# Optimization experiments

Measured on AMD Instinct MI355X. Metric: run time of the kernel, lower is better.

The kernel has to match this reference:

```python
import jax, jax.numpy as jnp
import numpy as np
import math

HIDDEN = 1024
N_HEADS = 16
N_KV = 4
HEAD_DIM = HIDDEN // N_HEADS  # 64
B, S = 2, 2048
THETA = 100000.0


def _freqs_cos_sin(dim, end, theta):
    # yarn params: original_max_position_embeddings=2048 >= end, so no ramp scaling,
    # attention_factor=1.0 -> plain RoPE frequencies.
    inv = 1.0 / theta ** (np.arange(0, dim, 2)[: dim // 2] / dim)
    t = np.arange(end)
    f = np.outer(t, inv).astype(np.float32)  # (end, dim/2)
    cos = np.concatenate([np.cos(f), np.cos(f)], axis=-1)  # (end, dim)
    sin = np.concatenate([np.sin(f), np.sin(f)], axis=-1)
    return jnp.asarray(cos), jnp.asarray(sin)


def _rotate(x):
    # stack([-x[...,1::2], x[...,::2]], -1).reshape_as(x)
    return jnp.stack([-x[..., 1::2], x[..., ::2]], axis=-1).reshape(x.shape)


def setup_inputs() -> dict:
    key = jax.random.key(0)
    ks = jax.random.split(key, 9)
    s = 0.02
    return {
        "hidden_states": jax.random.normal(ks[0], (B, S, HIDDEN), jnp.float32),
        "attention_mask": jnp.ones((B, S), jnp.int32),
        "Wq": jax.random.normal(ks[1], (HIDDEN, HIDDEN), jnp.float32) * s,
        "bq": jnp.zeros((HIDDEN,), jnp.float32),
        "Wk": jax.random.normal(ks[2], (HIDDEN, N_KV * HEAD_DIM), jnp.float32) * s,
        "bk": jnp.zeros((N_KV * HEAD_DIM,), jnp.float32),
        "Wv": jax.random.normal(ks[3], (HIDDEN, N_KV * HEAD_DIM), jnp.float32) * s,
        "bv": jnp.zeros((N_KV * HEAD_DIM,), jnp.float32),
        "Wo": jax.random.normal(ks[4], (HIDDEN, HIDDEN), jnp.float32) * s,
        "bo": jnp.zeros((HIDDEN,), jnp.float32),
    }


def reference(hidden_states, attention_mask, Wq, bq, Wk, bk, Wv, bv, Wo, bo):
    b, s, _ = hidden_states.shape
    q = (hidden_states @ Wq + bq).reshape(b, s, N_HEADS, HEAD_DIM)
    k = (hidden_states @ Wk + bk).reshape(b, s, N_KV, HEAD_DIM)
    v = (hidden_states @ Wv + bv).reshape(b, s, N_KV, HEAD_DIM)

    cos, sin = _freqs_cos_sin(HEAD_DIM, s, THETA)
    cos = cos[:, None, :]  # (s,1,d) broadcasts over (b,s,h,d)
    sin = sin[:, None, :]
    q = q * cos + _rotate(q) * sin
    k = k * cos + _rotate(k) * sin

    # GQA: repeat_interleave kv heads -> jnp.repeat along head axis
    rep = N_HEADS // N_KV
    k = jnp.repeat(k, rep, axis=2)
    v = jnp.repeat(v, rep, axis=2)

    scores = jnp.einsum("bqhd,bkhd->bhqk", q, k) / math.sqrt(HEAD_DIM)
    neg = jnp.finfo(scores.dtype).min
    causal = jnp.triu(jnp.ones((s, s), bool), k=1)  # (q,kv)
    bias = jnp.where(causal, neg, 0.0).astype(scores.dtype)[None, None]
    key_mask = attention_mask.astype(bool)[:, None, None, :]  # (b,1,1,kv)
    bias = jnp.where(key_mask, bias, neg)
    probs = jax.nn.softmax(scores + bias, axis=-1)
    attn = jnp.einsum("bhqk,bkhd->bqhd", probs, v).reshape(b, s, HIDDEN)
    return attn @ Wo + bo
```

## Files before the change

kernel.cpp:

```cpp
#include <hip/hip_runtime.h>
#include <cstddef>
#include <cstdint>

#define B_   2
#define S_   2048
#define HID  1024
#define NH_  16
#define NKV_ 4
#define DH_  64
#define ROWS (B_ * S_)
#define NQKV 1536
#define QSCALE 0.18033688011112042f

typedef __bf16 bf16_t;
typedef _Float16 f16_t;
typedef bf16_t bf16x8 __attribute__((ext_vector_type(8)));
typedef bf16_t bf16x4 __attribute__((ext_vector_type(4)));
typedef f16_t  f16x8  __attribute__((ext_vector_type(8)));
typedef f16_t  f16x4  __attribute__((ext_vector_type(4)));
typedef float  f32x4  __attribute__((ext_vector_type(4)));

typedef __attribute__((address_space(1))) const uint32_t gu32_t;
typedef __attribute__((address_space(3))) uint32_t lu32_t;

__device__ __forceinline__ void gl_lds16(const void* g, void* l) {
  __builtin_amdgcn_global_load_lds((gu32_t*)g, (lu32_t*)l, 16, 0, 0);
}

__global__ void prep_all(const float* __restrict__ hs,
                         const float* __restrict__ Wq, const float* __restrict__ Wk,
                         const float* __restrict__ Wv, const float* __restrict__ Wo,
                         const float* __restrict__ bq, const float* __restrict__ bk,
                         const float* __restrict__ bv,
                         bf16_t* __restrict__ hsb,
                         bf16_t* __restrict__ Wt, bf16_t* __restrict__ Wot,
                         float* __restrict__ ball, float2* __restrict__ lut)
{
  const int bid = blockIdx.x;
  if (bid < 2048) {
    const int i = (bid * 256 + threadIdx.x) * 8;
    float4 a = *(const float4*)(hs + i);
    float4 b = *(const float4*)(hs + i + 4);
    bf16x8 o;
    o[0]=(bf16_t)a.x; o[1]=(bf16_t)a.y; o[2]=(bf16_t)a.z; o[3]=(bf16_t)a.w;
    o[4]=(bf16_t)b.x; o[5]=(bf16_t)b.y; o[6]=(bf16_t)b.z; o[7]=(bf16_t)b.w;
    *(bf16x8*)(hsb + i) = o;
    return;
  }
  if (bid >= 4614) {
    const int idx = (bid - 4614) * 256 + threadIdx.x;
    const int s = idx >> 5, j = idx & 31;
    const float L = 0.51905126482615037f;
    const float ang = (float)s * exp2f(-L * (float)j);
    lut[idx] = make_float2(cosf(ang), sinf(ang));
    return;
  }
  if (bid >= 4608) {
    int i = (bid - 4608) * 256 + threadIdx.x;
    if (i < NQKV) ball[i] = (i < 1024) ? bq[i] : ((i < 1280) ? bk[i-1024] : bv[i-1280]);
    return;
  }
  const int wb = bid - 2048;
  const float* src; bf16_t* dst; int N, n0, k0;
  if (wb < 1024)      { src = Wq; dst = Wt;            N = 1024; int t = wb;      n0=(t&31)*32; k0=(t>>5)*32; }
  else if (wb < 1280) { src = Wk; dst = Wt + 1024*HID; N = 256;  int t = wb-1024; n0=(t&7)*32;  k0=(t>>3)*32; }
  else if (wb < 1536) { src = Wv; dst = Wt + 1280*HID; N = 256;  int t = wb-1280; n0=(t&7)*32;  k0=(t>>3)*32; }
  else                { src = Wo; dst = Wot;           N = 1024; int t = wb-1536; n0=(t&31)*32; k0=(t>>5)*32; }
  __shared__ bf16_t T[32][33];
  const int tx = threadIdx.x & 31, ty = threadIdx.x >> 5;
#pragma unroll
  for (int i = 0; i < 4; ++i)
    T[ty + i*8][tx] = (bf16_t)src[(size_t)(k0 + ty + i*8) * N + n0 + tx];
  __syncthreads();
#pragma unroll
  for (int i = 0; i < 4; ++i)
    dst[(size_t)(n0 + ty + i*8) * HID + k0 + tx] = T[tx][ty + i*8];
}

__global__ __launch_bounds__(256, 3) void gemm64_b16o(
    const bf16_t* __restrict__ A, const bf16_t* __restrict__ Bt,
    const float* __restrict__ bias, bf16_t* __restrict__ C, int N)
{
  __shared__ bf16_t As[128 * 64];
  __shared__ bf16_t Bs[64 * 64];
  const int tid  = threadIdx.x;
  const int w    = tid >> 6;
  const int lane = tid & 63;
  const int m    = lane & 15;
  const int quad = lane >> 4;
  const int wm   = w >> 1, wn = w & 1;
  const size_t bm = (size_t)blockIdx.y * 128;
  const size_t bn = (size_t)blockIdx.x * 64;

  const int srow = w * 8 + (lane >> 3);
  const int scol = (lane & 7) * 8;
  const bf16_t* Ag = A  + (bm + srow) * HID + scol;
  const bf16_t* Bg = Bt + (bn + srow) * HID + scol;

  f32x4 acc[4][2];
#pragma unroll
  for (int i = 0; i < 4; ++i)
#pragma unroll
    for (int j = 0; j < 2; ++j) acc[i][j] = (f32x4){0.f, 0.f, 0.f, 0.f};

  for (int k0 = 0; k0 < HID; k0 += 64) {
    __syncthreads();
#pragma unroll
    for (int i = 0; i < 4; ++i)
      gl_lds16(Ag + (size_t)(i * 32) * HID + k0, &As[(w * 8 + i * 32) * 64]);
#pragma unroll
    for (int i = 0; i < 2; ++i)
      gl_lds16(Bg + (size_t)(i * 32) * HID + k0, &Bs[(w * 8 + i * 32) * 64]);
    __syncthreads();
#pragma unroll
    for (int ks = 0; ks < 2; ++ks) {
      bf16x8 af[4], bfr[2];
#pragma unroll
      for (int mt = 0; mt < 4; ++mt)
        af[mt] = *(const bf16x8*)&As[(wm * 64 + mt * 16 + m) * 64 + ks * 32 + quad * 8];
#pragma unroll
      for (int nt = 0; nt < 2; ++nt)
        bfr[nt] = *(const bf16x8*)&Bs[(wn * 32 + nt * 16 + m) * 64 + ks * 32 + quad * 8];
#pragma unroll
      for (int mt = 0; mt < 4; ++mt)
#pragma unroll
        for (int nt = 0; nt < 2; ++nt)
          acc[mt][nt] = __builtin_amdgcn_mfma_f32_16x16x32_bf16(bfr[nt], af[mt], acc[mt][nt], 0, 0, 0);
    }
  }
#pragma unroll
  for (int mt = 0; mt < 4; ++mt) {
    const size_t row = bm + wm * 64 + mt * 16 + m;
#pragma unroll
    for (int nt = 0; nt < 2; ++nt) {
      const size_t col = bn + wn * 32 + nt * 16 + quad * 4;
      float4 bb = *(const float4*)&bias[col];
      bf16x4 o;
      o[0] = (bf16_t)(acc[mt][nt][0] + bb.x);
      o[1] = (bf16_t)(acc[mt][nt][1] + bb.y);
      o[2] = (bf16_t)(acc[mt][nt][2] + bb.z);
      o[3] = (bf16_t)(acc[mt][nt][3] + bb.w);
      *(bf16x4*)&C[row * N + col] = o;
    }
  }
}

__global__ __launch_bounds__(256, 3) void gemm64_f32o(
    const bf16_t* __restrict__ A, const bf16_t* __restrict__ Bt,
    const float* __restrict__ bias, float* __restrict__ C, int N)
{
  __shared__ bf16_t As[128 * 64];
  __shared__ bf16_t Bs[64 * 64];
  const int tid  = threadIdx.x;
  const int w    = tid >> 6;
  const int lane = tid & 63;
  const int m    = lane & 15;
  const int quad = lane >> 4;
  const int wm   = w >> 1, wn = w & 1;
  const size_t bm = (size_t)blockIdx.y * 128;
  const size_t bn = (size_t)blockIdx.x * 64;

  const int srow = w * 8 + (lane >> 3);
  const int scol = (lane & 7) * 8;
  const bf16_t* Ag = A  + (bm + srow) * HID + scol;
  const bf16_t* Bg = Bt + (bn + srow) * HID + scol;

  f32x4 acc[4][2];
#pragma unroll
  for (int i = 0; i < 4; ++i)
#pragma unroll
    for (int j = 0; j < 2; ++j) acc[i][j] = (f32x4){0.f, 0.f, 0.f, 0.f};

  for (int k0 = 0; k0 < HID; k0 += 64) {
    __syncthreads();
#pragma unroll
    for (int i = 0; i < 4; ++i)
      gl_lds16(Ag + (size_t)(i * 32) * HID + k0, &As[(w * 8 + i * 32) * 64]);
#pragma unroll
    for (int i = 0; i < 2; ++i)
      gl_lds16(Bg + (size_t)(i * 32) * HID + k0, &Bs[(w * 8 + i * 32) * 64]);
    __syncthreads();
#pragma unroll
    for (int ks = 0; ks < 2; ++ks) {
      bf16x8 af[4], bfr[2];
#pragma unroll
      for (int mt = 0; mt < 4; ++mt)
        af[mt] = *(const bf16x8*)&As[(wm * 64 + mt * 16 + m) * 64 + ks * 32 + quad * 8];
#pragma unroll
      for (int nt = 0; nt < 2; ++nt)
        bfr[nt] = *(const bf16x8*)&Bs[(wn * 32 + nt * 16 + m) * 64 + ks * 32 + quad * 8];
#pragma unroll
      for (int mt = 0; mt < 4; ++mt)
#pragma unroll
        for (int nt = 0; nt < 2; ++nt)
          acc[mt][nt] = __builtin_amdgcn_mfma_f32_16x16x32_bf16(bfr[nt], af[mt], acc[mt][nt], 0, 0, 0);
    }
  }
#pragma unroll
  for (int mt = 0; mt < 4; ++mt) {
    const size_t row = bm + wm * 64 + mt * 16 + m;
#pragma unroll
    for (int nt = 0; nt < 2; ++nt) {
      const size_t col = bn + wn * 32 + nt * 16 + quad * 4;
      float4 bb = *(const float4*)&bias[col];
      float4 o;
      o.x = acc[mt][nt][0] + bb.x; o.y = acc[mt][nt][1] + bb.y;
      o.z = acc[mt][nt][2] + bb.z; o.w = acc[mt][nt][3] + bb.w;
      *(float4*)&C[row * N + col] = o;
    }
  }
}

__global__ void prep_kv(const bf16_t* __restrict__ QKVb, const float2* __restrict__ lut,
                        bf16_t* __restrict__ Kimg, f16_t* __restrict__ Vimg)
{
  __shared__ bf16_t Lk[64][72];
  __shared__ bf16_t Lv[64][72];
  const int bid = blockIdx.x, t = threadIdx.x;
  const int kt = bid & 31, kvh = (bid >> 5) & 3, b = bid >> 7;
  const size_t img = ((size_t)(b * NKV_ + kvh) * 32 + kt) * 4096;

  {
    const int r0 = t >> 3, c8 = (t & 7) * 8;
#pragma unroll
    for (int i = 0; i < 2; ++i) {
      const int r = r0 + i * 32;
      const bf16_t* src = QKVb + (size_t)(b * S_ + kt * 64 + r) * NQKV + 1024 + kvh * DH_ + c8;
      *(bf16x8*)&Lk[r][c8] = *(const bf16x8*)src;
      *(bf16x8*)&Lv[r][c8] = *(const bf16x8*)(src + 256);
    }
  }
  __syncthreads();
  {
    const int key = t & 63, cg = t >> 6;
    const int srow = kt * 64 + key;
    bf16x8 a = *(const bf16x8*)&Lk[key][cg * 16];
    bf16x8 c = *(const bf16x8*)&Lk[key][cg * 16 + 8];
    const float2* lp = lut + srow * 32 + ((cg & 1) * 16);
    float v[16];
#pragma unroll
    for (int i = 0; i < 8; ++i) { v[i] = (float)a[i]; v[i + 8] = (float)c[i]; }
    bf16x8 o0, o1;
#pragma unroll
    for (int j = 0; j < 8; ++j) {
      const float2 ce = lp[2 * j], co = lp[2 * j + 1];
      const float y0 = v[2*j] * ce.x - v[2*j+1] * ce.y;
      const float y1 = v[2*j+1] * co.x + v[2*j] * co.y;
      if (j < 4) { o0[2*j] = (bf16_t)y0; o0[2*j+1] = (bf16_t)y1; }
      else       { o1[2*(j-4)] = (bf16_t)y0; o1[2*(j-4)+1] = (bf16_t)y1; }
    }
    const int s0 = (2 * cg) ^ (key & 7);
    *(bf16x8*)&Kimg[img + key * 64 + s0 * 8]       = o0;
    *(bf16x8*)&Kimg[img + key * 64 + (s0 ^ 1) * 8] = o1;
  }
  {
    const int d = t & 63, cg = t >> 6;
#pragma unroll
    for (int g4 = 0; g4 < 4; ++g4) {
      const int g = cg * 4 + g4;
      f16x4 o;
#pragma unroll
      for (int j = 0; j < 4; ++j)
        o[j] = (f16_t)(float)Lv[g * 4 + j][d];
      const int slot = g ^ (d & 15);
      *(f16x4*)&Vimg[img + d * 64 + slot * 4] = o;
    }
  }
}

__global__ __launch_bounds__(256, 2) void attn_v4(
    const bf16_t* __restrict__ QKVb, const float2* __restrict__ lut,
    const bf16_t* __restrict__ Kt2, const f16_t* __restrict__ Vt2,
    const int* __restrict__ amask, bf16_t* __restrict__ Ab)
{
  __shared__ __align__(16) bf16_t Ks[64 * 64];
  __shared__ __align__(16) f16_t  Vs[64 * 64];

  const int tid  = threadIdx.x;
  const int w    = tid >> 6;
  const int lane = tid & 63;
  const int m    = lane & 15;
  const int quad = lane >> 4;
  const int h    = blockIdx.y;
  const int b    = blockIdx.z;
  const int kvh  = h >> 2;
  const int bx   = blockIdx.x;
  const int qt   = (w == 0) ? 2*bx : (w == 1) ? 2*bx + 1 : (w == 2) ? 62 - 2*bx : 63 - 2*bx;
  const int q0w  = qt * 32;
  const int qlast = q0w + 31;
  const int nkt  = 32 - bx;

  bf16x8 aq[2][2];
#pragma unroll
  for (int mt = 0; mt < 2; ++mt) {
    const int spos = q0w + mt * 16 + m;
    const bf16_t* qsrc = QKVb + (size_t)(b * S_ + spos) * NQKV + h * DH_;
    float2 l8[8];
#pragma unroll
    for (int j = 0; j < 8; ++j) l8[j] = lut[spos * 32 + quad * 8 + j];
#pragma unroll
    for (int kc = 0; kc < 2; ++kc) {
      bf16x8 x = *(const bf16x8*)(qsrc + kc * 32 + quad * 8);
      bf16x8 y;
#pragma unroll
      for (int i = 0; i < 4; ++i) {
        const float x0 = (float)x[2*i], x1 = (float)x[2*i+1];
        y[2*i]   = (bf16_t)((x0 * l8[2*i].x   - x1 * l8[2*i].y)   * QSCALE);
        y[2*i+1] = (bf16_t)((x1 * l8[2*i+1].x + x0 * l8[2*i+1].y) * QSCALE);
      }
      aq[mt][kc] = y;
    }
  }

  f32x4 oacc[2][4];
#pragma unroll
  for (int mt = 0; mt < 2; ++mt)
#pragma unroll
    for (int d = 0; d < 4; ++d) oacc[mt][d] = (f32x4){0.f,0.f,0.f,0.f};
  float lp[2] = {0.f, 0.f};

  const size_t imgbase = ((size_t)(b * NKV_ + kvh) * 32) * 4096;
  const bf16_t* Kg = Kt2 + imgbase;
  const f16_t*  Vg = Vt2 + imgbase;
  const int x0s = quad ^ (m & 7);
  const int x1s = (4 + quad) ^ (m & 7);
  const int* amp = amask + b * S_;

  for (int kt = 0; kt < nkt; ++kt) {
    const int kbase = kt * 64;
    __syncthreads();
    gl_lds16(Kg + (size_t)kt * 4096 + (2*w)   * 512 + lane * 8, &Ks[(2*w)   * 512]);
    gl_lds16(Kg + (size_t)kt * 4096 + (2*w+1) * 512 + lane * 8, &Ks[(2*w+1) * 512]);
    gl_lds16(Vg + (size_t)kt * 4096 + (2*w)   * 512 + lane * 8, &Vs[(2*w)   * 512]);
    gl_lds16(Vg + (size_t)kt * 4096 + (2*w+1) * 512 + lane * 8, &Vs[(2*w+1) * 512]);
    __syncthreads();
    if (kbase > qlast) continue;

    const uint64_t mb = __ballot(amp[kbase + lane] != 0);

    f32x4 sc[2][4];
#pragma unroll
    for (int mt = 0; mt < 2; ++mt)
#pragma unroll
      for (int cb = 0; cb < 4; ++cb) sc[mt][cb] = (f32x4){0.f,0.f,0.f,0.f};
#pragma unroll
    for (int cb = 0; cb < 4; ++cb) {
      const bf16x8 bk0 = *(const bf16x8*)&Ks[(cb*16 + m) * 64 + x0s * 8];
      const bf16x8 bk1 = *(const bf16x8*)&Ks[(cb*16 + m) * 64 + x1s * 8];
#pragma unroll
      for (int mt = 0; mt < 2; ++mt) {
        sc[mt][cb] = __builtin_amdgcn_mfma_f32_16x16x32_bf16(bk0, aq[mt][0], sc[mt][cb], 0, 0, 0);
        sc[mt][cb] = __builtin_amdgcn_mfma_f32_16x16x32_bf16(bk1, aq[mt][1], sc[mt][cb], 0, 0, 0);
      }
    }

    f16x4 bp[2][4];
#pragma unroll
    for (int mt = 0; mt < 2; ++mt) {
      const bool needm = (kbase + 63 > q0w + mt*16) || (mb != ~0ull);
      if (needm) {
        const int qv = q0w + mt*16 + m;
#pragma unroll
        for (int cb = 0; cb < 4; ++cb)
#pragma unroll
          for (int r = 0; r < 4; ++r) {
            const int idx = cb*16 + quad*4 + r;
            const bool ok = (kbase + idx <= qv) && ((mb >> idx) & 1);
            sc[mt][cb][r] = ok ? sc[mt][cb][r] : -1e38f;
          }
      }
      float sum = 0.f;
#pragma unroll
      for (int cb = 0; cb < 4; ++cb) {
        f16x4 pp;
#pragma unroll
        for (int r = 0; r < 4; ++r) {
          const float p = exp2f(sc[mt][cb][r]);
          sum += p;
          pp[r] = (f16_t)p;
        }
        bp[mt][cb] = pp;
      }
      lp[mt] += sum;
    }

#pragma unroll
    for (int cb = 0; cb < 4; ++cb) {
      f16x4 av[4];
#pragma unroll
      for (int dblk = 0; dblk < 4; ++dblk) {
        const int slot = (cb * 4 + quad) ^ m;
        av[dblk] = *(const f16x4*)&Vs[(dblk*16 + m) * 64 + slot * 4];
      }
#pragma unroll
      for (int mt = 0; mt < 2; ++mt)
#pragma unroll
        for (int dblk = 0; dblk < 4; ++dblk)
          oacc[mt][dblk] = __builtin_amdgcn_mfma_f32_16x16x16f16(av[dblk], bp[mt][cb], oacc[mt][dblk], 0, 0, 0);
    }
  }

#pragma unroll
  for (int mt = 0; mt < 2; ++mt) {
    float l = lp[mt];
    l += __shfl_xor(l, 16);
    l += __shfl_xor(l, 32);
    const float inv = 1.0f / l;
    const size_t row = (size_t)(b * S_ + q0w + mt*16 + m);
#pragma unroll
    for (int dblk = 0; dblk < 4; ++dblk) {
      bf16x4 o;
      o[0] = (bf16_t)(oacc[mt][dblk][0] * inv);
      o[1] = (bf16_t)(oacc[mt][dblk][1] * inv);
      o[2] = (bf16_t)(oacc[mt][dblk][2] * inv);
      o[3] = (bf16_t)(oacc[mt][dblk][3] * inv);
      *(bf16x4*)&Ab[row * HID + h * DH_ + dblk * 16 + quad * 4] = o;
    }
  }
}

extern "C" void kernel_launch(void* const* d_in, const int* in_sizes, int n_in,
                              void* d_out, int out_size, void* d_ws, size_t ws_size,
                              hipStream_t stream)
{
  const float* hs    = (const float*)d_in[0];
  const int*   amask = (const int*)  d_in[1];
  const float* Wq    = (const float*)d_in[2];
  const float* bq    = (const float*)d_in[3];
  const float* Wk    = (const float*)d_in[4];
  const float* bk    = (const float*)d_in[5];
  const float* Wv    = (const float*)d_in[6];
  const float* bv    = (const float*)d_in[7];
  const float* Wo    = (const float*)d_in[8];
  const float* bo    = (const float*)d_in[9];
  float* out = (float*)d_out;

  bf16_t* QKVb = (bf16_t*)d_ws;
  bf16_t* hsb  = QKVb + (size_t)ROWS * NQKV;
  bf16_t* Wt   = hsb + (size_t)ROWS * HID;
  bf16_t* Wot  = Wt + (size_t)NQKV * HID;
  float*  ball = (float*)(Wot + (size_t)HID * HID);
  bf16_t* Kimg = (bf16_t*)(ball + NQKV);
  f16_t*  Vimg = (f16_t*)(Kimg + (size_t)B_*NKV_*32*4096);
  float2* lut  = (float2*)(Vimg + (size_t)B_*NKV_*32*4096);
  bf16_t* Ab   = hsb;

  prep_all<<<4870, 256, 0, stream>>>(hs, Wq, Wk, Wv, Wo, bq, bk, bv,
                                     hsb, Wt, Wot, ball, lut);

  gemm64_b16o<<<dim3(NQKV/64, ROWS/128), 256, 0, stream>>>(hsb, Wt, ball, QKVb, NQKV);

  prep_kv<<<256, 256, 0, stream>>>(QKVb, lut, Kimg, Vimg);

  attn_v4<<<dim3(16, NH_, B_), 256, 0, stream>>>(QKVb, lut, Kimg, Vimg, amask, Ab);

  gemm64_f32o<<<dim3(HID/64, ROWS/128), 256, 0, stream>>>(Ab, Wot, bo, out, HID);
}
```

Measured before the change: 208.7 us.

## Split attention into single-wave blocks, one per 32-query tile

The attention kernel moves from 256-thread blocks, where four waves share K/V tiles with causal load balancing, to 64-thread single-wave blocks that each handle one 32-query tile. Each wave loads its own K/V tile into LDS and waits with s_waitcnt instead of block barriers, and blocks are launched heaviest-first. This removes __syncthreads stalls and the idle wave iterations caused by uneven causal work, at the cost of up to four times more redundant K/V global-to-LDS traffic and a loss of shared-tile reuse.

Result: no change. 212.7 us (+1.9%).

```diff
diff --git a/kernel.cpp b/kernel.cpp
--- a/kernel.cpp
+++ b/kernel.cpp
@@ -268,7 +268,7 @@
   }
 }
 
-__global__ __launch_bounds__(256, 2) void attn_v4(
+__global__ __launch_bounds__(64) void attn_v5(
     const bf16_t* __restrict__ QKVb, const float2* __restrict__ lut,
     const bf16_t* __restrict__ Kt2, const f16_t* __restrict__ Vt2,
     const int* __restrict__ amask, bf16_t* __restrict__ Ab)
@@ -276,19 +276,15 @@
   __shared__ __align__(16) bf16_t Ks[64 * 64];
   __shared__ __align__(16) f16_t  Vs[64 * 64];
 
-  const int tid  = threadIdx.x;
-  const int w    = tid >> 6;
-  const int lane = tid & 63;
+  const int lane = threadIdx.x;
   const int m    = lane & 15;
   const int quad = lane >> 4;
   const int h    = blockIdx.y;
   const int b    = blockIdx.z;
   const int kvh  = h >> 2;
-  const int bx   = blockIdx.x;
-  const int qt   = (w == 0) ? 2*bx : (w == 1) ? 2*bx + 1 : (w == 2) ? 62 - 2*bx : 63 - 2*bx;
+  const int qt   = 63 - blockIdx.x;
   const int q0w  = qt * 32;
-  const int qlast = q0w + 31;
-  const int nkt  = 32 - bx;
+  const int nkt  = ((q0w + 31) >> 6) + 1;
 
   bf16x8 aq[2][2];
 #pragma unroll
@@ -317,7 +313,7 @@
   for (int mt = 0; mt < 2; ++mt)
 #pragma unroll
     for (int d = 0; d < 4; ++d) oacc[mt][d] = (f32x4){0.f,0.f,0.f,0.f};
-  float lp[2] = {0.f, 0.f};
+  float lpart[2] = {0.f, 0.f};
 
   const size_t imgbase = ((size_t)(b * NKV_ + kvh) * 32) * 4096;
   const bf16_t* Kg = Kt2 + imgbase;
@@ -328,15 +324,15 @@
 
   for (int kt = 0; kt < nkt; ++kt) {
     const int kbase = kt * 64;
-    __syncthreads();
-    gl_lds16(Kg + (size_t)kt * 4096 + (2*w)   * 512 + lane * 8, &Ks[(2*w)   * 512]);
-    gl_lds16(Kg + (size_t)kt * 4096 + (2*w+1) * 512 + lane * 8, &Ks[(2*w+1) * 512]);
-    gl_lds16(Vg + (size_t)kt * 4096 + (2*w)   * 512 + lane * 8, &Vs[(2*w)   * 512]);
-    gl_lds16(Vg + (size_t)kt * 4096 + (2*w+1) * 512 + lane * 8, &Vs[(2*w+1) * 512]);
-    __syncthreads();
-    if (kbase > qlast) continue;
+#pragma unroll
+    for (int i = 0; i < 8; ++i)
+      gl_lds16(Kg + (size_t)kt * 4096 + i * 512 + lane * 8, &Ks[i * 512]);
+#pragma unroll
+    for (int i = 0; i < 8; ++i)
+      gl_lds16(Vg + (size_t)kt * 4096 + i * 512 + lane * 8, &Vs[i * 512]);
 
     const uint64_t mb = __ballot(amp[kbase + lane] != 0);
+    __builtin_amdgcn_s_waitcnt(0x0F70);
 
     f32x4 sc[2][4];
 #pragma unroll
@@ -381,7 +377,7 @@
         }
         bp[mt][cb] = pp;
       }
-      lp[mt] += sum;
+      lpart[mt] += sum;
     }
 
 #pragma unroll
@@ -402,7 +398,7 @@
 
 #pragma unroll
   for (int mt = 0; mt < 2; ++mt) {
-    float l = lp[mt];
+    float l = lpart[mt];
     l += __shfl_xor(l, 16);
     l += __shfl_xor(l, 32);
     const float inv = 1.0f / l;
@@ -452,7 +448,7 @@
 
   prep_kv<<<256, 256, 0, stream>>>(QKVb, lut, Kimg, Vimg);
 
-  attn_v4<<<dim3(16, NH_, B_), 256, 0, stream>>>(QKVb, lut, Kimg, Vimg, amask, Ab);
+  attn_v5<<<dim3(64, NH_, B_), 64, 0, stream>>>(QKVb, lut, Kimg, Vimg, amask, Ab);
 
   gemm64_f32o<<<dim3(HID/64, ROWS/128), 256, 0, stream>>>(Ab, Wot, bo, out, HID);
 }
```
